# Optimization experiments

Hardware: AMD Instinct MI355X
Metric: run time of the kernel (lower is better)

Reference implementation:

```python
import jax, jax.numpy as jnp
import numpy as np

N = 50000      # nodes
E = 800000     # edges (avg degree 16)
D = 64         # input/hidden dim
OUT = 1        # output head dim
ATT_SLOPE = 0.2   # PyG GATConv leaky_relu slope for attention logits
ACT_SLOPE = 0.01  # nn.LeakyReLU default slope


def _gat_layer(x, src, dst, W, a_src, a_dst, b, n):
    """PyG GATConv, heads=1, concat=True, with self-loops already in src/dst."""
    h = x @ W.T                                   # [n, D]
    logit = jax.nn.leaky_relu(h[src] @ a_src + h[dst] @ a_dst, ATT_SLOPE)  # [e]
    m = jax.ops.segment_max(logit, dst, num_segments=n)                    # per-dst max
    e = jnp.exp(logit - m[dst])
    denom = jax.ops.segment_sum(e, dst, num_segments=n)
    coef = e / denom[dst]                         # softmax over incoming edges
    out = jax.ops.segment_sum(coef[:, None] * h[src], dst, num_segments=n)
    return out + b


def setup_inputs() -> dict:
    key = jax.random.key(0)
    ks = jax.random.split(key, 16)
    s = 1.0 / np.sqrt(D)
    inp = {"x": jax.random.normal(ks[0], (N, D), dtype=jnp.float32)}
    for i in range(3):
        inp[f"W{i}"] = jax.random.normal(ks[1 + 4 * i], (D, D), dtype=jnp.float32) * s
        inp[f"a_src{i}"] = jax.random.normal(ks[2 + 4 * i], (D,), dtype=jnp.float32) * s
        inp[f"a_dst{i}"] = jax.random.normal(ks[3 + 4 * i], (D,), dtype=jnp.float32) * s
        inp[f"b{i}"] = jnp.zeros((D,), dtype=jnp.float32)
    inp["Wout"] = jax.random.normal(ks[13], (OUT, D), dtype=jnp.float32) * s
    inp["bout"] = jnp.zeros((OUT,), dtype=jnp.float32)
    inp["edge_index"] = jax.random.randint(ks[14], (2, E), 0, N, dtype=jnp.int64)
    return inp


def reference(x, W0, a_src0, a_dst0, b0, W1, a_src1, a_dst1, b1,
              W2, a_src2, a_dst2, b2, Wout, bout, edge_index):
    n = x.shape[0]
    loops = jnp.arange(n, dtype=edge_index.dtype)
    src = jnp.concatenate([edge_index[0], loops])  # GATConv add_self_loops=True
    dst = jnp.concatenate([edge_index[1], loops])
    act = lambda v: jax.nn.leaky_relu(v, ACT_SLOPE)
    h = act(_gat_layer(x, src, dst, W0, a_src0, a_dst0, b0, n))
    h = act(_gat_layer(h, src, dst, W1, a_src1, a_dst1, b1, n))
    h = act(_gat_layer(h, src, dst, W2, a_src2, a_dst2, b2, n))
    return h @ Wout.T + bout                       # [n, OUT]
```

## Files before the change

kernel.cpp:

```cpp
#include <hip/hip_runtime.h>
#include <hip/hip_fp16.h>

#define DD 64
#define ATT_SLOPE 0.2f
#define ACT_SLOPE 0.01f
#define GNPB 32
#define RCAP 64
#define PA_CHUNK 2048
#define BSH 8
#define BNODES 256
#define BCAP 5888

template <bool IN_HALF>
__device__ __forceinline__ void gemm_body(
        const void* __restrict__ in_, const float* __restrict__ W,
        const float* __restrict__ a_src, const float* __restrict__ a_dst,
        __half* __restrict__ h, float* __restrict__ as_out,
        float* __restrict__ ad_out, int n_nodes, int base, float* xin) {
    int t = threadIdx.x;
    int lane = t & 63;
    int w = t >> 6;
    if (IN_HALF) {
        const uint2* src = (const uint2*)in_;
        float4* xin4 = (float4*)xin;
        int lim = n_nodes * (DD / 4);
        #pragma unroll
        for (int i = 0; i < 2; ++i) {
            int idx = i * 256 + t;
            int gi = base * (DD / 4) + idx;
            uint2 v = {0, 0};
            if (gi < lim) v = src[gi];
            float2 f0 = __half22float2(*(const __half2*)&v.x);
            float2 f1 = __half22float2(*(const __half2*)&v.y);
            xin4[idx] = make_float4(f0.x, f0.y, f1.x, f1.y);
        }
    } else {
        float4* xin4 = (float4*)xin;
        const float4* src4 = (const float4*)in_;
        int lim = n_nodes * (DD / 4);
        #pragma unroll
        for (int i = 0; i < (GNPB * DD / 4) / 256; ++i) {
            int idx = i * 256 + t;
            int gi = base * (DD / 4) + idx;
            xin4[idx] = (gi < lim) ? src4[gi]
                                   : make_float4(0.f, 0.f, 0.f, 0.f);
        }
    }
    __syncthreads();

    int n0 = base + w * 8;
    if (n0 >= n_nodes) return;

    float asl = a_src[lane], adl = a_dst[lane];
    const float* wrow = W + (size_t)lane * 64;
    int rmax = n_nodes - n0; if (rmax > 8) rmax = 8;

    if (rmax == 8) {
        float a[8] = {0.f, 0.f, 0.f, 0.f, 0.f, 0.f, 0.f, 0.f};
        #pragma unroll
        for (int kq = 0; kq < 16; ++kq) {
            float4 wv = *(const float4*)(wrow + kq * 4);
            #pragma unroll
            for (int r = 0; r < 8; ++r) {
                float4 xv = *(const float4*)&xin[(w * 8 + r) * DD + kq * 4];
                a[r] = fmaf(xv.x, wv.x, a[r]); a[r] = fmaf(xv.y, wv.y, a[r]);
                a[r] = fmaf(xv.z, wv.z, a[r]); a[r] = fmaf(xv.w, wv.w, a[r]);
            }
        }
        #pragma unroll
        for (int r = 0; r < 8; ++r)
            h[(size_t)(n0 + r) * 64 + lane] = __float2half(a[r]);
        float s[16];
        #pragma unroll
        for (int r = 0; r < 8; ++r) { s[2 * r] = a[r] * asl; s[2 * r + 1] = a[r] * adl; }
        #pragma unroll
        for (int m = 32; m >= 1; m >>= 1) {
            #pragma unroll
            for (int i = 0; i < 16; ++i) s[i] += __shfl_xor(s[i], m, 64);
        }
        if (lane == 0) {
            #pragma unroll
            for (int r = 0; r < 8; ++r) {
                as_out[n0 + r] = s[2 * r];
                ad_out[n0 + r] = s[2 * r + 1];
            }
        }
    } else {
        for (int r = 0; r < rmax; ++r) {
            int node = n0 + r;
            float acc = 0.f;
            #pragma unroll
            for (int kq = 0; kq < 16; ++kq) {
                float4 wv = *(const float4*)(wrow + kq * 4);
                float4 xv = *(const float4*)&xin[(w * 8 + r) * DD + kq * 4];
                acc = fmaf(xv.x, wv.x, acc); acc = fmaf(xv.y, wv.y, acc);
                acc = fmaf(xv.z, wv.z, acc); acc = fmaf(xv.w, wv.w, acc);
            }
            h[(size_t)node * 64 + lane] = __float2half(acc);
            float s1 = acc * asl, s2 = acc * adl;
            #pragma unroll
            for (int m = 32; m >= 1; m >>= 1) {
                s1 += __shfl_xor(s1, m, 64);
                s2 += __shfl_xor(s2, m, 64);
            }
            if (lane == 0) { as_out[node] = s1; ad_out[node] = s2; }
        }
    }
}

__global__ __launch_bounds__(256) void gemm0_binA_kernel(
        const float* __restrict__ x, const float* __restrict__ W,
        const float* __restrict__ a_src, const float* __restrict__ a_dst,
        __half* __restrict__ h, float* __restrict__ as_out,
        float* __restrict__ ad_out, int n_nodes,
        const int* __restrict__ ei, int E,
        int* __restrict__ bcur, unsigned int* __restrict__ bucket_buf,
        int bin_blocks) {
    __shared__ float xin[GNPB * DD];
    int* hist  = (int*)xin;
    int* gbase = hist + 256;
    int bid = blockIdx.x;
    if (bid >= bin_blocks) {
        gemm_body<false>(x, W, a_src, a_dst, h, as_out, ad_out, n_nodes,
                         (bid - bin_blocks) * GNPB, xin);
        return;
    }
    int t = threadIdx.x;
    int base_e = bid * PA_CHUNK;
    int ET = E + n_nodes;
    hist[t] = 0;
    __syncthreads();

    unsigned int ent[8];
    short eb[8];
    short ep[8];
    #pragma unroll
    for (int j = 0; j < 8; ++j) {
        int e = base_e + j * 256 + t;
        eb[j] = -1;
        if (e >= ET) continue;
        int s, d;
        if (e < E) { s = ei[e]; d = ei[E + e]; }
        else       { s = e - E; d = s; }
        int b = d >> BSH;
        ent[j] = (unsigned int)s | ((unsigned int)(d & (BNODES - 1)) << 16);
        eb[j] = (short)b;
        ep[j] = (short)atomicAdd(&hist[b], 1);
    }
    __syncthreads();
    {
        int c = hist[t];
        gbase[t] = (c > 0) ? atomicAdd(&bcur[t], c) : 0;
    }
    __syncthreads();
    #pragma unroll
    for (int j = 0; j < 8; ++j) {
        if (eb[j] < 0) continue;
        int pos = gbase[eb[j]] + ep[j];
        if (pos < BCAP) bucket_buf[(size_t)eb[j] * BCAP + pos] = ent[j];
    }
}

__global__ __launch_bounds__(256) void binB_kernel(
        const unsigned int* __restrict__ bucket_buf, const int* __restrict__ bcur,
        int* __restrict__ counts, unsigned short* __restrict__ col_src,
        int n_nodes) {
    __shared__ int cur[BNODES];
    int b = blockIdx.x, t = threadIdx.x;
    if (t < BNODES) cur[t] = 0;
    __syncthreads();
    int cnt = bcur[b]; if (cnt > BCAP) cnt = BCAP;
    const unsigned int* buf = bucket_buf + (size_t)b * BCAP;
    for (int i = t; i < cnt; i += 256) {
        unsigned int en = buf[i];
        int s = en & 0xFFFF;
        int dl = en >> 16;
        int pos = atomicAdd(&cur[dl], 1);
        if (pos < RCAP)
            col_src[(((b << BSH) + dl) << 6) + pos] = (unsigned short)s;
    }
    __syncthreads();
    int n0 = b << BSH;
    if (t < BNODES) {
        int d = n0 + t;
        if (d < n_nodes) counts[d] = cur[t];
    }
}

__global__ __launch_bounds__(256) void gemm_alpha_kernel(
        const __half* __restrict__ in, const float* __restrict__ W,
        const float* __restrict__ a_src, const float* __restrict__ a_dst,
        __half* __restrict__ h, float* __restrict__ as_out,
        float* __restrict__ ad_out, int n_nodes) {
    __shared__ float xin[GNPB * DD];
    gemm_body<true>(in, W, a_src, a_dst, h, as_out, ad_out, n_nodes,
                    blockIdx.x * GNPB, xin);
}

template <bool FUSE_HEAD>
__global__ __launch_bounds__(256) void aggregate_kernel(
        const int* __restrict__ counts, const unsigned short* __restrict__ col_src,
        const __half* __restrict__ h, const float* __restrict__ as_arr,
        const float* __restrict__ ad_arr, const float* __restrict__ b,
        __half* __restrict__ out16, float* __restrict__ head_out,
        const float* __restrict__ Wout, const float* __restrict__ bout,
        int n_nodes) {
    int t = threadIdx.x;
    int lane = t & 63;
    int w = t >> 6;
    int g = lane >> 3, u = lane & 7;
    int node = blockIdx.x * GNPB + w * 8 + g;
    bool valid = node < n_nodes;

    int cnt = 0; float adn = 0.f;
    if (valid) { cnt = counts[node]; adn = ad_arr[node]; }
    if (cnt > RCAP) cnt = RCAP;
    const unsigned short* crow = col_src + ((size_t)node << 6);

    float acc[8] = {0.f, 0.f, 0.f, 0.f, 0.f, 0.f, 0.f, 0.f};
    float lsum = 0.f;

    int nb = (cnt + 7) >> 3;
    uint4 iv = make_uint4(0, 0, 0, 0);
    if (cnt > 0) iv = *(const uint4*)crow;

    for (int bi = 0; bi < nb; ++bi) {
        uint4 ivn = make_uint4(0, 0, 0, 0);
        if (bi + 1 < nb) ivn = *(const uint4*)(crow + (bi + 1) * 8);
        int rem = cnt - (bi << 3); if (rem > 8) rem = 8;

        int s0 = iv.x & 0xFFFF, s1 = iv.x >> 16;
        int s2 = iv.y & 0xFFFF, s3 = iv.y >> 16;
        int s4 = iv.z & 0xFFFF, s5 = iv.z >> 16;
        int s6 = iv.w & 0xFFFF, s7 = iv.w >> 16;
        int ss0 = s0, ss1 = s1, ss2 = s2, ss3 = s3;
        int ss4 = s4, ss5 = s5, ss6 = s6, ss7 = s7;

        uint4 r0={0,0,0,0},r1={0,0,0,0},r2={0,0,0,0},r3={0,0,0,0};
        uint4 r4={0,0,0,0},r5={0,0,0,0},r6={0,0,0,0},r7={0,0,0,0};
        float a0=0,a1=0,a2=0,a3=0,a4=0,a5=0,a6=0,a7=0;
        if (0 < rem) { a0 = as_arr[ss0]; r0 = *(const uint4*)(h + (size_t)ss0 * 64 + u * 8); }
        if (1 < rem) { a1 = as_arr[ss1]; r1 = *(const uint4*)(h + (size_t)ss1 * 64 + u * 8); }
        if (2 < rem) { a2 = as_arr[ss2]; r2 = *(const uint4*)(h + (size_t)ss2 * 64 + u * 8); }
        if (3 < rem) { a3 = as_arr[ss3]; r3 = *(const uint4*)(h + (size_t)ss3 * 64 + u * 8); }
        if (4 < rem) { a4 = as_arr[ss4]; r4 = *(const uint4*)(h + (size_t)ss4 * 64 + u * 8); }
        if (5 < rem) { a5 = as_arr[ss5]; r5 = *(const uint4*)(h + (size_t)ss5 * 64 + u * 8); }
        if (6 < rem) { a6 = as_arr[ss6]; r6 = *(const uint4*)(h + (size_t)ss6 * 64 + u * 8); }
        if (7 < rem) { a7 = as_arr[ss7]; r7 = *(const uint4*)(h + (size_t)ss7 * 64 + u * 8); }

        #define PROC(i, ri, ai)                                              \
        if (i < rem) {                                                       \
            float lg = ai + adn;                                             \
            lg = (lg >= 0.f) ? lg : ATT_SLOPE * lg;                          \
            float p = __expf(lg);                                            \
            lsum += p;                                                       \
            float2 f0 = __half22float2(*(const __half2*)&ri.x);              \
            float2 f1 = __half22float2(*(const __half2*)&ri.y);              \
            float2 f2 = __half22float2(*(const __half2*)&ri.z);              \
            float2 f3 = __half22float2(*(const __half2*)&ri.w);              \
            acc[0] = fmaf(p, f0.x, acc[0]); acc[1] = fmaf(p, f0.y, acc[1]);  \
            acc[2] = fmaf(p, f1.x, acc[2]); acc[3] = fmaf(p, f1.y, acc[3]);  \
            acc[4] = fmaf(p, f2.x, acc[4]); acc[5] = fmaf(p, f2.y, acc[5]);  \
            acc[6] = fmaf(p, f3.x, acc[6]); acc[7] = fmaf(p, f3.y, acc[7]);  \
        }
        PROC(0, r0, a0) PROC(1, r1, a1) PROC(2, r2, a2) PROC(3, r3, a3)
        PROC(4, r4, a4) PROC(5, r5, a5) PROC(6, r6, a6) PROC(7, r7, a7)
        #undef PROC
        iv = ivn;
    }

    float inv = 1.f / lsum;
    const float4 b0 = *(const float4*)(b + u * 8);
    const float4 b1 = *(const float4*)(b + u * 8 + 4);
    float o[8];
    o[0] = acc[0] * inv + b0.x; o[1] = acc[1] * inv + b0.y;
    o[2] = acc[2] * inv + b0.z; o[3] = acc[3] * inv + b0.w;
    o[4] = acc[4] * inv + b1.x; o[5] = acc[5] * inv + b1.y;
    o[6] = acc[6] * inv + b1.z; o[7] = acc[7] * inv + b1.w;
    #pragma unroll
    for (int i = 0; i < 8; ++i) o[i] = (o[i] >= 0.f) ? o[i] : ACT_SLOPE * o[i];

    if (FUSE_HEAD) {
        const float4 w0 = *(const float4*)(Wout + u * 8);
        const float4 w1 = *(const float4*)(Wout + u * 8 + 4);
        float pd = o[0] * w0.x + o[1] * w0.y + o[2] * w0.z + o[3] * w0.w
                 + o[4] * w1.x + o[5] * w1.y + o[6] * w1.z + o[7] * w1.w;
        pd += __shfl_xor(pd, 1, 64);
        pd += __shfl_xor(pd, 2, 64);
        pd += __shfl_xor(pd, 4, 64);
        if (valid && u == 0) head_out[node] = pd + bout[0];
    } else if (valid) {
        __half2 p0 = __floats2half2_rn(o[0], o[1]);
        __half2 p1 = __floats2half2_rn(o[2], o[3]);
        __half2 p2 = __floats2half2_rn(o[4], o[5]);
        __half2 p3 = __floats2half2_rn(o[6], o[7]);
        uint4 pv;
        pv.x = *(unsigned int*)&p0; pv.y = *(unsigned int*)&p1;
        pv.z = *(unsigned int*)&p2; pv.w = *(unsigned int*)&p3;
        *(uint4*)(out16 + ((size_t)node << 6) + u * 8) = pv;
    }
}


extern "C" void kernel_launch(void* const* d_in, const int* in_sizes, int n_in,
                              void* d_out, int out_size, void* d_ws, size_t ws_size,
                              hipStream_t stream) {
    const float* x     = (const float*)d_in[0];
    const float* W[3]  = {(const float*)d_in[1], (const float*)d_in[5], (const float*)d_in[9]};
    const float* as[3] = {(const float*)d_in[2], (const float*)d_in[6], (const float*)d_in[10]};
    const float* ad[3] = {(const float*)d_in[3], (const float*)d_in[7], (const float*)d_in[11]};
    const float* bv[3] = {(const float*)d_in[4], (const float*)d_in[8], (const float*)d_in[12]};
    const float* Wout  = (const float*)d_in[13];
    const float* bout  = (const float*)d_in[14];
    const int*   ei    = (const int*)d_in[15];

    const int N  = in_sizes[0] / DD;
    const int E  = in_sizes[15] / 2;
    const int ET = E + N;
    const int NBUCK = (N + BNODES - 1) >> BSH;

    char* ws = (char*)d_ws;
    size_t off = 0;
    auto alloc = [&](size_t bytes) {
        void* p = ws + off;
        off = (off + bytes + 255) & ~(size_t)255;
        return p;
    };
    unsigned short* col_src = (unsigned short*)alloc((size_t)N * RCAP * 2);
    int*    counts  = (int*)alloc((size_t)N * 4);
    int*    bcur    = (int*)alloc(256 * 4);
    float*  asA     = (float*)alloc((size_t)N * 4);
    float*  adA     = (float*)alloc((size_t)N * 4);
    float*  asB     = (float*)alloc((size_t)N * 4);
    float*  adB     = (float*)alloc((size_t)N * 4);
    __half* hA      = (__half*)alloc((size_t)N * DD * 2);
    __half* hB      = (__half*)alloc((size_t)N * DD * 2);
    __half* obuf16  = (__half*)alloc((size_t)N * DD * 2);
    unsigned int* bucket_buf = (unsigned int*)alloc((size_t)NBUCK * BCAP * 4);
    (void)ws_size;

    int gridG = (N + GNPB - 1) / GNPB;
    int nA    = (ET + PA_CHUNK - 1) / PA_CHUNK;

    hipMemsetAsync(bcur, 0, 256 * 4, stream);
    gemm0_binA_kernel<<<gridG + nA, 256, 0, stream>>>(
        x, W[0], as[0], ad[0], hA, asA, adA, N,
        ei, E, bcur, bucket_buf, nA);
    binB_kernel<<<NBUCK, 256, 0, stream>>>(bucket_buf, bcur, counts, col_src, N);

    aggregate_kernel<false><<<gridG, 256, 0, stream>>>(
        counts, col_src, hA, asA, adA, bv[0], obuf16,
        nullptr, nullptr, nullptr, N);
    gemm_alpha_kernel<<<gridG, 256, 0, stream>>>(obuf16, W[1], as[1], ad[1],
                                                 hB, asB, adB, N);
    aggregate_kernel<false><<<gridG, 256, 0, stream>>>(
        counts, col_src, hB, asB, adB, bv[1], obuf16,
        nullptr, nullptr, nullptr, N);
    gemm_alpha_kernel<<<gridG, 256, 0, stream>>>(obuf16, W[2], as[2], ad[2],
                                                 hA, asA, adA, N);
    aggregate_kernel<true><<<gridG, 256, 0, stream>>>(
        counts, col_src, hA, asA, adA, bv[2], nullptr,
        (float*)d_out, Wout, bout, N);
}
```

Baseline: 244.8 us.

## Fuse all GAT layers into one persistent cooperative kernel with grid syncs

Replaces the seven separate kernel launches (binning, GEMMs, aggregations) with one cooperative persistent kernel. Its blocks loop over tiles for each stage and use grid-wide syncs between stages. The aim is to remove launch overhead and inter-kernel gaps between the short stages. In exchange, occupancy is capped at the co-resident block count, and the aggregation stages lose the latency hiding that full-size grids with many more blocks provided.

```diff
diff --git a/kernel.cpp b/kernel.cpp
--- a/kernel.cpp
+++ b/kernel.cpp
@@ -1,5 +1,8 @@
 #include <hip/hip_runtime.h>
 #include <hip/hip_fp16.h>
+#include <hip/hip_cooperative_groups.h>
+
+namespace cg = cooperative_groups;
 
 #define DD 64
 #define ATT_SLOPE 0.2f
@@ -11,8 +14,9 @@
 #define BNODES 256
 #define BCAP 5888
 
+
 template <bool IN_HALF>
-__device__ __forceinline__ void gemm_body(
+__device__ __forceinline__ void gemm_tile(
         const void* __restrict__ in_, const float* __restrict__ W,
         const float* __restrict__ a_src, const float* __restrict__ a_dst,
         __half* __restrict__ h, float* __restrict__ as_out,
@@ -49,84 +53,74 @@
     __syncthreads();
 
     int n0 = base + w * 8;
-    if (n0 >= n_nodes) return;
-
-    float asl = a_src[lane], adl = a_dst[lane];
-    const float* wrow = W + (size_t)lane * 64;
-    int rmax = n_nodes - n0; if (rmax > 8) rmax = 8;
-
-    if (rmax == 8) {
-        float a[8] = {0.f, 0.f, 0.f, 0.f, 0.f, 0.f, 0.f, 0.f};
-        #pragma unroll
-        for (int kq = 0; kq < 16; ++kq) {
-            float4 wv = *(const float4*)(wrow + kq * 4);
-            #pragma unroll
-            for (int r = 0; r < 8; ++r) {
-                float4 xv = *(const float4*)&xin[(w * 8 + r) * DD + kq * 4];
-                a[r] = fmaf(xv.x, wv.x, a[r]); a[r] = fmaf(xv.y, wv.y, a[r]);
-                a[r] = fmaf(xv.z, wv.z, a[r]); a[r] = fmaf(xv.w, wv.w, a[r]);
-            }
-        }
-        #pragma unroll
-        for (int r = 0; r < 8; ++r)
-            h[(size_t)(n0 + r) * 64 + lane] = __float2half(a[r]);
-        float s[16];
-        #pragma unroll
-        for (int r = 0; r < 8; ++r) { s[2 * r] = a[r] * asl; s[2 * r + 1] = a[r] * adl; }
-        #pragma unroll
-        for (int m = 32; m >= 1; m >>= 1) {
-            #pragma unroll
-            for (int i = 0; i < 16; ++i) s[i] += __shfl_xor(s[i], m, 64);
-        }
-        if (lane == 0) {
-            #pragma unroll
-            for (int r = 0; r < 8; ++r) {
-                as_out[n0 + r] = s[2 * r];
-                ad_out[n0 + r] = s[2 * r + 1];
-            }
-        }
-    } else {
-        for (int r = 0; r < rmax; ++r) {
-            int node = n0 + r;
-            float acc = 0.f;
+    if (n0 < n_nodes) {
+        float asl = a_src[lane], adl = a_dst[lane];
+        const float* wrow = W + (size_t)lane * 64;
+        int rmax = n_nodes - n0; if (rmax > 8) rmax = 8;
+
+        if (rmax == 8) {
+            float a[8] = {0.f, 0.f, 0.f, 0.f, 0.f, 0.f, 0.f, 0.f};
             #pragma unroll
             for (int kq = 0; kq < 16; ++kq) {
                 float4 wv = *(const float4*)(wrow + kq * 4);
-                float4 xv = *(const float4*)&xin[(w * 8 + r) * DD + kq * 4];
-                acc = fmaf(xv.x, wv.x, acc); acc = fmaf(xv.y, wv.y, acc);
-                acc = fmaf(xv.z, wv.z, acc); acc = fmaf(xv.w, wv.w, acc);
+                #pragma unroll
+                for (int r = 0; r < 8; ++r) {
+                    float4 xv = *(const float4*)&xin[(w * 8 + r) * DD + kq * 4];
+                    a[r] = fmaf(xv.x, wv.x, a[r]); a[r] = fmaf(xv.y, wv.y, a[r]);
+                    a[r] = fmaf(xv.z, wv.z, a[r]); a[r] = fmaf(xv.w, wv.w, a[r]);
+                }
             }
-            h[(size_t)node * 64 + lane] = __float2half(acc);
-            float s1 = acc * asl, s2 = acc * adl;
+            #pragma unroll
+            for (int r = 0; r < 8; ++r)
+                h[(size_t)(n0 + r) * 64 + lane] = __float2half(a[r]);
+            float s[16];
+            #pragma unroll
+            for (int r = 0; r < 8; ++r) { s[2*r] = a[r] * asl; s[2*r+1] = a[r] * adl; }
             #pragma unroll
             for (int m = 32; m >= 1; m >>= 1) {
-                s1 += __shfl_xor(s1, m, 64);
-                s2 += __shfl_xor(s2, m, 64);
+                #pragma unroll
+                for (int i = 0; i < 16; ++i) s[i] += __shfl_xor(s[i], m, 64);
             }
-            if (lane == 0) { as_out[node] = s1; ad_out[node] = s2; }
+            if (lane == 0) {
+                #pragma unroll
+                for (int r = 0; r < 8; ++r) {
+                    as_out[n0 + r] = s[2 * r];
+                    ad_out[n0 + r] = s[2 * r + 1];
+                }
+            }
+        } else {
+            for (int r = 0; r < rmax; ++r) {
+                int node = n0 + r;
+                float acc = 0.f;
+                #pragma unroll
+                for (int kq = 0; kq < 16; ++kq) {
+                    float4 wv = *(const float4*)(wrow + kq * 4);
+                    float4 xv = *(const float4*)&xin[(w * 8 + r) * DD + kq * 4];
+                    acc = fmaf(xv.x, wv.x, acc); acc = fmaf(xv.y, wv.y, acc);
+                    acc = fmaf(xv.z, wv.z, acc); acc = fmaf(xv.w, wv.w, acc);
+                }
+                h[(size_t)node * 64 + lane] = __float2half(acc);
+                float s1 = acc * asl, s2 = acc * adl;
+                #pragma unroll
+                for (int m = 32; m >= 1; m >>= 1) {
+                    s1 += __shfl_xor(s1, m, 64);
+                    s2 += __shfl_xor(s2, m, 64);
+                }
+                if (lane == 0) { as_out[node] = s1; ad_out[node] = s2; }
+            }
         }
     }
-}
-
-__global__ __launch_bounds__(256) void gemm0_binA_kernel(
-        const float* __restrict__ x, const float* __restrict__ W,
-        const float* __restrict__ a_src, const float* __restrict__ a_dst,
-        __half* __restrict__ h, float* __restrict__ as_out,
-        float* __restrict__ ad_out, int n_nodes,
-        const int* __restrict__ ei, int E,
+    __syncthreads();
+}
+
+__device__ __forceinline__ void binA_task(
+        const int* __restrict__ ei, int E, int n_nodes,
         int* __restrict__ bcur, unsigned int* __restrict__ bucket_buf,
-        int bin_blocks) {
-    __shared__ float xin[GNPB * DD];
+        int chunk, float* xin) {
     int* hist  = (int*)xin;
     int* gbase = hist + 256;
-    int bid = blockIdx.x;
-    if (bid >= bin_blocks) {
-        gemm_body<false>(x, W, a_src, a_dst, h, as_out, ad_out, n_nodes,
-                         (bid - bin_blocks) * GNPB, xin);
-        return;
-    }
     int t = threadIdx.x;
-    int base_e = bid * PA_CHUNK;
+    int base_e = chunk * PA_CHUNK;
     int ET = E + n_nodes;
     hist[t] = 0;
     __syncthreads();
@@ -159,15 +153,16 @@
         int pos = gbase[eb[j]] + ep[j];
         if (pos < BCAP) bucket_buf[(size_t)eb[j] * BCAP + pos] = ent[j];
     }
-}
-
-__global__ __launch_bounds__(256) void binB_kernel(
+    __syncthreads();
+}
+
+__device__ __forceinline__ void binB_task(
         const unsigned int* __restrict__ bucket_buf, const int* __restrict__ bcur,
         int* __restrict__ counts, unsigned short* __restrict__ col_src,
-        int n_nodes) {
-    __shared__ int cur[BNODES];
-    int b = blockIdx.x, t = threadIdx.x;
-    if (t < BNODES) cur[t] = 0;
+        int n_nodes, int b, float* xin) {
+    int* cur = (int*)xin;
+    int t = threadIdx.x;
+    cur[t] = 0;
     __syncthreads();
     int cnt = bcur[b]; if (cnt > BCAP) cnt = BCAP;
     const unsigned int* buf = bucket_buf + (size_t)b * BCAP;
@@ -181,35 +176,26 @@
     }
     __syncthreads();
     int n0 = b << BSH;
-    if (t < BNODES) {
+    {
         int d = n0 + t;
         if (d < n_nodes) counts[d] = cur[t];
     }
-}
-
-__global__ __launch_bounds__(256) void gemm_alpha_kernel(
-        const __half* __restrict__ in, const float* __restrict__ W,
-        const float* __restrict__ a_src, const float* __restrict__ a_dst,
-        __half* __restrict__ h, float* __restrict__ as_out,
-        float* __restrict__ ad_out, int n_nodes) {
-    __shared__ float xin[GNPB * DD];
-    gemm_body<true>(in, W, a_src, a_dst, h, as_out, ad_out, n_nodes,
-                    blockIdx.x * GNPB, xin);
+    __syncthreads();
 }
 
 template <bool FUSE_HEAD>
-__global__ __launch_bounds__(256) void aggregate_kernel(
+__device__ __forceinline__ void agg_tile(
         const int* __restrict__ counts, const unsigned short* __restrict__ col_src,
         const __half* __restrict__ h, const float* __restrict__ as_arr,
         const float* __restrict__ ad_arr, const float* __restrict__ b,
         __half* __restrict__ out16, float* __restrict__ head_out,
         const float* __restrict__ Wout, const float* __restrict__ bout,
-        int n_nodes) {
+        int n_nodes, int tile) {
     int t = threadIdx.x;
     int lane = t & 63;
     int w = t >> 6;
     int g = lane >> 3, u = lane & 7;
-    int node = blockIdx.x * GNPB + w * 8 + g;
+    int node = tile * GNPB + w * 8 + g;
     bool valid = node < n_nodes;
 
     int cnt = 0; float adn = 0.f;
@@ -229,12 +215,10 @@
         if (bi + 1 < nb) ivn = *(const uint4*)(crow + (bi + 1) * 8);
         int rem = cnt - (bi << 3); if (rem > 8) rem = 8;
 
-        int s0 = iv.x & 0xFFFF, s1 = iv.x >> 16;
-        int s2 = iv.y & 0xFFFF, s3 = iv.y >> 16;
-        int s4 = iv.z & 0xFFFF, s5 = iv.z >> 16;
-        int s6 = iv.w & 0xFFFF, s7 = iv.w >> 16;
-        int ss0 = s0, ss1 = s1, ss2 = s2, ss3 = s3;
-        int ss4 = s4, ss5 = s5, ss6 = s6, ss7 = s7;
+        int ss0 = iv.x & 0xFFFF, ss1 = iv.x >> 16;
+        int ss2 = iv.y & 0xFFFF, ss3 = iv.y >> 16;
+        int ss4 = iv.z & 0xFFFF, ss5 = iv.z >> 16;
+        int ss6 = iv.w & 0xFFFF, ss7 = iv.w >> 16;
 
         uint4 r0={0,0,0,0},r1={0,0,0,0},r2={0,0,0,0},r3={0,0,0,0};
         uint4 r4={0,0,0,0},r5={0,0,0,0},r6={0,0,0,0},r7={0,0,0,0};
@@ -301,22 +285,91 @@
     }
 }
 
+__global__ __launch_bounds__(256, 4) void gnn_persistent(
+        const float* __restrict__ x,
+        const float* __restrict__ W0, const float* __restrict__ as0,
+        const float* __restrict__ ad0, const float* __restrict__ b0,
+        const float* __restrict__ W1, const float* __restrict__ as1,
+        const float* __restrict__ ad1, const float* __restrict__ b1,
+        const float* __restrict__ W2, const float* __restrict__ as2,
+        const float* __restrict__ ad2, const float* __restrict__ b2,
+        const float* __restrict__ Wout, const float* __restrict__ bout,
+        const int* __restrict__ ei, int E, int n_nodes,
+        int* bcur, unsigned int* bucket_buf,
+        int* counts, unsigned short* col_src,
+        float* asA, float* adA, float* asB, float* adB,
+        __half* hA, __half* hB, __half* obuf16,
+        float* head_out) {
+    __shared__ float xin[GNPB * DD];
+    cg::grid_group grid = cg::this_grid();
+    const int nbk   = gridDim.x;
+    const int bid   = blockIdx.x;
+    const int gridG = (n_nodes + GNPB - 1) / GNPB;
+    const int nA    = (E + n_nodes + PA_CHUNK - 1) / PA_CHUNK;
+    const int NBUCK = (n_nodes + BNODES - 1) >> BSH;
+
+    int tasks0 = nA + gridG;
+    for (int task = bid; task < tasks0; task += nbk) {
+        if (task < nA)
+            binA_task(ei, E, n_nodes, bcur, bucket_buf, task, xin);
+        else
+            gemm_tile<false>(x, W0, as0, ad0, hA, asA, adA, n_nodes,
+                             (task - nA) * GNPB, xin);
+    }
+    grid.sync();
+
+    for (int bkt = bid; bkt < NBUCK; bkt += nbk)
+        binB_task(bucket_buf, bcur, counts, col_src, n_nodes, bkt, xin);
+    grid.sync();
+
+    for (int tile = bid; tile < gridG; tile += nbk)
+        agg_tile<false>(counts, col_src, hA, asA, adA, b0, obuf16,
+                        nullptr, nullptr, nullptr, n_nodes, tile);
+    grid.sync();
+
+    for (int tile = bid; tile < gridG; tile += nbk)
+        gemm_tile<true>(obuf16, W1, as1, ad1, hB, asB, adB, n_nodes,
+                        tile * GNPB, xin);
+    grid.sync();
+
+    for (int tile = bid; tile < gridG; tile += nbk)
+        agg_tile<false>(counts, col_src, hB, asB, adB, b1, obuf16,
+                        nullptr, nullptr, nullptr, n_nodes, tile);
+    grid.sync();
+
+    for (int tile = bid; tile < gridG; tile += nbk)
+        gemm_tile<true>(obuf16, W2, as2, ad2, hA, asA, adA, n_nodes,
+                        tile * GNPB, xin);
+    grid.sync();
+
+    for (int tile = bid; tile < gridG; tile += nbk)
+        agg_tile<true>(counts, col_src, hA, asA, adA, b2,
+                       nullptr, head_out, Wout, bout, n_nodes, tile);
+}
+
 
 extern "C" void kernel_launch(void* const* d_in, const int* in_sizes, int n_in,
                               void* d_out, int out_size, void* d_ws, size_t ws_size,
                               hipStream_t stream) {
     const float* x     = (const float*)d_in[0];
-    const float* W[3]  = {(const float*)d_in[1], (const float*)d_in[5], (const float*)d_in[9]};
-    const float* as[3] = {(const float*)d_in[2], (const float*)d_in[6], (const float*)d_in[10]};
-    const float* ad[3] = {(const float*)d_in[3], (const float*)d_in[7], (const float*)d_in[11]};
-    const float* bv[3] = {(const float*)d_in[4], (const float*)d_in[8], (const float*)d_in[12]};
+    const float* W0    = (const float*)d_in[1];
+    const float* as0   = (const float*)d_in[2];
+    const float* ad0   = (const float*)d_in[3];
+    const float* b0    = (const float*)d_in[4];
+    const float* W1    = (const float*)d_in[5];
+    const float* as1   = (const float*)d_in[6];
+    const float* ad1   = (const float*)d_in[7];
+    const float* b1    = (const float*)d_in[8];
+    const float* W2    = (const float*)d_in[9];
+    const float* as2   = (const float*)d_in[10];
+    const float* ad2   = (const float*)d_in[11];
+    const float* b2    = (const float*)d_in[12];
     const float* Wout  = (const float*)d_in[13];
     const float* bout  = (const float*)d_in[14];
     const int*   ei    = (const int*)d_in[15];
 
-    const int N  = in_sizes[0] / DD;
-    const int E  = in_sizes[15] / 2;
-    const int ET = E + N;
+    int N  = in_sizes[0] / DD;
+    int E  = in_sizes[15] / 2;
     const int NBUCK = (N + BNODES - 1) >> BSH;
 
     char* ws = (char*)d_ws;
@@ -337,28 +390,43 @@
     __half* hB      = (__half*)alloc((size_t)N * DD * 2);
     __half* obuf16  = (__half*)alloc((size_t)N * DD * 2);
     unsigned int* bucket_buf = (unsigned int*)alloc((size_t)NBUCK * BCAP * 4);
+    float* head_out = (float*)d_out;
     (void)ws_size;
 
     int gridG = (N + GNPB - 1) / GNPB;
-    int nA    = (ET + PA_CHUNK - 1) / PA_CHUNK;
+    int nA    = (E + N + PA_CHUNK - 1) / PA_CHUNK;
+    int tasks0 = nA + gridG;
+
+    static int capBlocks = 0;
+    if (capBlocks == 0) {
+        int nbPerCU = 0;
+        hipOccupancyMaxActiveBlocksPerMultiprocessor(
+            &nbPerCU, (const void*)gnn_persistent, 256, 0);
+        if (nbPerCU < 1) nbPerCU = 1;
+        int dev = 0;
+        hipGetDevice(&dev);
+        hipDeviceProp_t prop;
+        hipGetDeviceProperties(&prop, dev);
+        int cus = prop.multiProcessorCount > 0 ? prop.multiProcessorCount : 256;
+        capBlocks = nbPerCU * cus;
+    }
+    int grid = tasks0 < capBlocks ? tasks0 : capBlocks;
 
     hipMemsetAsync(bcur, 0, 256 * 4, stream);
-    gemm0_binA_kernel<<<gridG + nA, 256, 0, stream>>>(
-        x, W[0], as[0], ad[0], hA, asA, adA, N,
-        ei, E, bcur, bucket_buf, nA);
-    binB_kernel<<<NBUCK, 256, 0, stream>>>(bucket_buf, bcur, counts, col_src, N);
-
-    aggregate_kernel<false><<<gridG, 256, 0, stream>>>(
-        counts, col_src, hA, asA, adA, bv[0], obuf16,
-        nullptr, nullptr, nullptr, N);
-    gemm_alpha_kernel<<<gridG, 256, 0, stream>>>(obuf16, W[1], as[1], ad[1],
-                                                 hB, asB, adB, N);
-    aggregate_kernel<false><<<gridG, 256, 0, stream>>>(
-        counts, col_src, hB, asB, adB, bv[1], obuf16,
-        nullptr, nullptr, nullptr, N);
-    gemm_alpha_kernel<<<gridG, 256, 0, stream>>>(obuf16, W[2], as[2], ad[2],
-                                                 hA, asA, adA, N);
-    aggregate_kernel<true><<<gridG, 256, 0, stream>>>(
-        counts, col_src, hA, asA, adA, bv[2], nullptr,
-        (float*)d_out, Wout, bout, N);
-}
+
+    void* args[] = {
+        (void*)&x,
+        (void*)&W0, (void*)&as0, (void*)&ad0, (void*)&b0,
+        (void*)&W1, (void*)&as1, (void*)&ad1, (void*)&b1,
+        (void*)&W2, (void*)&as2, (void*)&ad2, (void*)&b2,
+        (void*)&Wout, (void*)&bout,
+        (void*)&ei, (void*)&E, (void*)&N,
+        (void*)&bcur, (void*)&bucket_buf,
+        (void*)&counts, (void*)&col_src,
+        (void*)&asA, (void*)&adA, (void*)&asB, (void*)&adB,
+        (void*)&hA, (void*)&hB, (void*)&obuf16,
+        (void*)&head_out
+    };
+    hipLaunchCooperativeKernel((const void*)gnn_persistent,
+                               dim3(grid), dim3(256), args, 0, stream);
+}
```

New measurement: 644.7 us. 163% more time.

## Fuse aggregation with next layer's linear transform and attention projections

Applied to the files above, without the earlier changes.

Merges each intermediate aggregate kernel with the following GEMM+alpha kernel. The aggregated node features go straight into shared memory and feed the next layer's W multiply, so the fp16 intermediate buffer is neither written nor re-read. This also drops two kernel launches. The fused kernel keeps features in fp32 instead of rounding to half between stages, and it may raise register pressure or lower occupancy in the aggregation phase.

```diff
diff --git a/kernel.cpp b/kernel.cpp
--- a/kernel.cpp
+++ b/kernel.cpp
@@ -11,40 +11,24 @@
 #define BNODES 256
 #define BCAP 5888
 
-template <bool IN_HALF>
-__device__ __forceinline__ void gemm_body(
-        const void* __restrict__ in_, const float* __restrict__ W,
+
+__device__ __forceinline__ void gemm_body0(
+        const float* __restrict__ in, const float* __restrict__ W,
         const float* __restrict__ a_src, const float* __restrict__ a_dst,
         __half* __restrict__ h, float* __restrict__ as_out,
         float* __restrict__ ad_out, int n_nodes, int base, float* xin) {
     int t = threadIdx.x;
     int lane = t & 63;
     int w = t >> 6;
-    if (IN_HALF) {
-        const uint2* src = (const uint2*)in_;
-        float4* xin4 = (float4*)xin;
-        int lim = n_nodes * (DD / 4);
-        #pragma unroll
-        for (int i = 0; i < 2; ++i) {
-            int idx = i * 256 + t;
-            int gi = base * (DD / 4) + idx;
-            uint2 v = {0, 0};
-            if (gi < lim) v = src[gi];
-            float2 f0 = __half22float2(*(const __half2*)&v.x);
-            float2 f1 = __half22float2(*(const __half2*)&v.y);
-            xin4[idx] = make_float4(f0.x, f0.y, f1.x, f1.y);
-        }
-    } else {
-        float4* xin4 = (float4*)xin;
-        const float4* src4 = (const float4*)in_;
-        int lim = n_nodes * (DD / 4);
-        #pragma unroll
-        for (int i = 0; i < (GNPB * DD / 4) / 256; ++i) {
-            int idx = i * 256 + t;
-            int gi = base * (DD / 4) + idx;
-            xin4[idx] = (gi < lim) ? src4[gi]
-                                   : make_float4(0.f, 0.f, 0.f, 0.f);
-        }
+    float4* xin4 = (float4*)xin;
+    const float4* src4 = (const float4*)in;
+    int lim = n_nodes * (DD / 4);
+    #pragma unroll
+    for (int i = 0; i < (GNPB * DD / 4) / 256; ++i) {
+        int idx = i * 256 + t;
+        int gi = base * (DD / 4) + idx;
+        xin4[idx] = (gi < lim) ? src4[gi]
+                               : make_float4(0.f, 0.f, 0.f, 0.f);
     }
     __syncthreads();
 
@@ -121,8 +105,8 @@
     int* gbase = hist + 256;
     int bid = blockIdx.x;
     if (bid >= bin_blocks) {
-        gemm_body<false>(x, W, a_src, a_dst, h, as_out, ad_out, n_nodes,
-                         (bid - bin_blocks) * GNPB, xin);
+        gemm_body0(x, W, a_src, a_dst, h, as_out, ad_out, n_nodes,
+                   (bid - bin_blocks) * GNPB, xin);
         return;
     }
     int t = threadIdx.x;
@@ -187,31 +171,12 @@
     }
 }
 
-__global__ __launch_bounds__(256) void gemm_alpha_kernel(
-        const __half* __restrict__ in, const float* __restrict__ W,
-        const float* __restrict__ a_src, const float* __restrict__ a_dst,
-        __half* __restrict__ h, float* __restrict__ as_out,
-        float* __restrict__ ad_out, int n_nodes) {
-    __shared__ float xin[GNPB * DD];
-    gemm_body<true>(in, W, a_src, a_dst, h, as_out, ad_out, n_nodes,
-                    blockIdx.x * GNPB, xin);
-}
-
-template <bool FUSE_HEAD>
-__global__ __launch_bounds__(256) void aggregate_kernel(
+__device__ __forceinline__ bool agg_core(
         const int* __restrict__ counts, const unsigned short* __restrict__ col_src,
         const __half* __restrict__ h, const float* __restrict__ as_arr,
         const float* __restrict__ ad_arr, const float* __restrict__ b,
-        __half* __restrict__ out16, float* __restrict__ head_out,
-        const float* __restrict__ Wout, const float* __restrict__ bout,
-        int n_nodes) {
-    int t = threadIdx.x;
-    int lane = t & 63;
-    int w = t >> 6;
-    int g = lane >> 3, u = lane & 7;
-    int node = blockIdx.x * GNPB + w * 8 + g;
+        int n_nodes, int node, int u, float o[8]) {
     bool valid = node < n_nodes;
-
     int cnt = 0; float adn = 0.f;
     if (valid) { cnt = counts[node]; adn = ad_arr[node]; }
     if (cnt > RCAP) cnt = RCAP;
@@ -229,12 +194,10 @@
         if (bi + 1 < nb) ivn = *(const uint4*)(crow + (bi + 1) * 8);
         int rem = cnt - (bi << 3); if (rem > 8) rem = 8;
 
-        int s0 = iv.x & 0xFFFF, s1 = iv.x >> 16;
-        int s2 = iv.y & 0xFFFF, s3 = iv.y >> 16;
-        int s4 = iv.z & 0xFFFF, s5 = iv.z >> 16;
-        int s6 = iv.w & 0xFFFF, s7 = iv.w >> 16;
-        int ss0 = s0, ss1 = s1, ss2 = s2, ss3 = s3;
-        int ss4 = s4, ss5 = s5, ss6 = s6, ss7 = s7;
+        int ss0 = iv.x & 0xFFFF, ss1 = iv.x >> 16;
+        int ss2 = iv.y & 0xFFFF, ss3 = iv.y >> 16;
+        int ss4 = iv.z & 0xFFFF, ss5 = iv.z >> 16;
+        int ss6 = iv.w & 0xFFFF, ss7 = iv.w >> 16;
 
         uint4 r0={0,0,0,0},r1={0,0,0,0},r2={0,0,0,0},r3={0,0,0,0};
         uint4 r4={0,0,0,0},r5={0,0,0,0},r6={0,0,0,0},r7={0,0,0,0};
@@ -272,33 +235,123 @@
     float inv = 1.f / lsum;
     const float4 b0 = *(const float4*)(b + u * 8);
     const float4 b1 = *(const float4*)(b + u * 8 + 4);
-    float o[8];
     o[0] = acc[0] * inv + b0.x; o[1] = acc[1] * inv + b0.y;
     o[2] = acc[2] * inv + b0.z; o[3] = acc[3] * inv + b0.w;
     o[4] = acc[4] * inv + b1.x; o[5] = acc[5] * inv + b1.y;
     o[6] = acc[6] * inv + b1.z; o[7] = acc[7] * inv + b1.w;
     #pragma unroll
     for (int i = 0; i < 8; ++i) o[i] = (o[i] >= 0.f) ? o[i] : ACT_SLOPE * o[i];
-
-    if (FUSE_HEAD) {
-        const float4 w0 = *(const float4*)(Wout + u * 8);
-        const float4 w1 = *(const float4*)(Wout + u * 8 + 4);
-        float pd = o[0] * w0.x + o[1] * w0.y + o[2] * w0.z + o[3] * w0.w
-                 + o[4] * w1.x + o[5] * w1.y + o[6] * w1.z + o[7] * w1.w;
-        pd += __shfl_xor(pd, 1, 64);
-        pd += __shfl_xor(pd, 2, 64);
-        pd += __shfl_xor(pd, 4, 64);
-        if (valid && u == 0) head_out[node] = pd + bout[0];
-    } else if (valid) {
-        __half2 p0 = __floats2half2_rn(o[0], o[1]);
-        __half2 p1 = __floats2half2_rn(o[2], o[3]);
-        __half2 p2 = __floats2half2_rn(o[4], o[5]);
-        __half2 p3 = __floats2half2_rn(o[6], o[7]);
-        uint4 pv;
-        pv.x = *(unsigned int*)&p0; pv.y = *(unsigned int*)&p1;
-        pv.z = *(unsigned int*)&p2; pv.w = *(unsigned int*)&p3;
-        *(uint4*)(out16 + ((size_t)node << 6) + u * 8) = pv;
-    }
+    return valid;
+}
+
+__global__ __launch_bounds__(256) void fused_agg_gemm_kernel(
+        const int* __restrict__ counts, const unsigned short* __restrict__ col_src,
+        const __half* __restrict__ h, const float* __restrict__ as_arr,
+        const float* __restrict__ ad_arr, const float* __restrict__ b,
+        const float* __restrict__ Wn, const float* __restrict__ an_src,
+        const float* __restrict__ an_dst, __half* __restrict__ h_next,
+        float* __restrict__ as_next, float* __restrict__ ad_next,
+        int n_nodes) {
+    __shared__ float xin[GNPB * DD];
+    int t = threadIdx.x;
+    int lane = t & 63;
+    int w = t >> 6;
+    int g = lane >> 3, u = lane & 7;
+    int node = blockIdx.x * GNPB + w * 8 + g;
+
+    float o[8];
+    bool valid = agg_core(counts, col_src, h, as_arr, ad_arr, b,
+                          n_nodes, node, u, o);
+    if (valid) {
+        float4* row = (float4*)&xin[(w * 8 + g) * DD + u * 8];
+        row[0] = make_float4(o[0], o[1], o[2], o[3]);
+        row[1] = make_float4(o[4], o[5], o[6], o[7]);
+    }
+    __syncthreads();
+
+    int n0 = blockIdx.x * GNPB + w * 8;
+    if (n0 >= n_nodes) return;
+    float asl = an_src[lane], adl = an_dst[lane];
+    const float* wrow = Wn + (size_t)lane * 64;
+    int rmax = n_nodes - n0; if (rmax > 8) rmax = 8;
+
+    if (rmax == 8) {
+        float a[8] = {0.f, 0.f, 0.f, 0.f, 0.f, 0.f, 0.f, 0.f};
+        #pragma unroll
+        for (int kq = 0; kq < 16; ++kq) {
+            float4 wv = *(const float4*)(wrow + kq * 4);
+            #pragma unroll
+            for (int r = 0; r < 8; ++r) {
+                float4 xv = *(const float4*)&xin[(w * 8 + r) * DD + kq * 4];
+                a[r] = fmaf(xv.x, wv.x, a[r]); a[r] = fmaf(xv.y, wv.y, a[r]);
+                a[r] = fmaf(xv.z, wv.z, a[r]); a[r] = fmaf(xv.w, wv.w, a[r]);
+            }
+        }
+        #pragma unroll
+        for (int r = 0; r < 8; ++r)
+            h_next[(size_t)(n0 + r) * 64 + lane] = __float2half(a[r]);
+        float s[16];
+        #pragma unroll
+        for (int r = 0; r < 8; ++r) { s[2 * r] = a[r] * asl; s[2 * r + 1] = a[r] * adl; }
+        #pragma unroll
+        for (int m = 32; m >= 1; m >>= 1) {
+            #pragma unroll
+            for (int i = 0; i < 16; ++i) s[i] += __shfl_xor(s[i], m, 64);
+        }
+        if (lane == 0) {
+            #pragma unroll
+            for (int r = 0; r < 8; ++r) {
+                as_next[n0 + r] = s[2 * r];
+                ad_next[n0 + r] = s[2 * r + 1];
+            }
+        }
+    } else {
+        for (int r = 0; r < rmax; ++r) {
+            int nd = n0 + r;
+            float acc = 0.f;
+            #pragma unroll
+            for (int kq = 0; kq < 16; ++kq) {
+                float4 wv = *(const float4*)(wrow + kq * 4);
+                float4 xv = *(const float4*)&xin[(w * 8 + r) * DD + kq * 4];
+                acc = fmaf(xv.x, wv.x, acc); acc = fmaf(xv.y, wv.y, acc);
+                acc = fmaf(xv.z, wv.z, acc); acc = fmaf(xv.w, wv.w, acc);
+            }
+            h_next[(size_t)nd * 64 + lane] = __float2half(acc);
+            float s1 = acc * asl, s2 = acc * adl;
+            #pragma unroll
+            for (int m = 32; m >= 1; m >>= 1) {
+                s1 += __shfl_xor(s1, m, 64);
+                s2 += __shfl_xor(s2, m, 64);
+            }
+            if (lane == 0) { as_next[nd] = s1; ad_next[nd] = s2; }
+        }
+    }
+}
+
+__global__ __launch_bounds__(256) void aggregate_head_kernel(
+        const int* __restrict__ counts, const unsigned short* __restrict__ col_src,
+        const __half* __restrict__ h, const float* __restrict__ as_arr,
+        const float* __restrict__ ad_arr, const float* __restrict__ b,
+        float* __restrict__ head_out, const float* __restrict__ Wout,
+        const float* __restrict__ bout, int n_nodes) {
+    int t = threadIdx.x;
+    int lane = t & 63;
+    int w = t >> 6;
+    int g = lane >> 3, u = lane & 7;
+    int node = blockIdx.x * GNPB + w * 8 + g;
+
+    float o[8];
+    bool valid = agg_core(counts, col_src, h, as_arr, ad_arr, b,
+                          n_nodes, node, u, o);
+
+    const float4 w0 = *(const float4*)(Wout + u * 8);
+    const float4 w1 = *(const float4*)(Wout + u * 8 + 4);
+    float pd = o[0] * w0.x + o[1] * w0.y + o[2] * w0.z + o[3] * w0.w
+             + o[4] * w1.x + o[5] * w1.y + o[6] * w1.z + o[7] * w1.w;
+    pd += __shfl_xor(pd, 1, 64);
+    pd += __shfl_xor(pd, 2, 64);
+    pd += __shfl_xor(pd, 4, 64);
+    if (valid && u == 0) head_out[node] = pd + bout[0];
 }
 
 
@@ -335,7 +388,6 @@
     float*  adB     = (float*)alloc((size_t)N * 4);
     __half* hA      = (__half*)alloc((size_t)N * DD * 2);
     __half* hB      = (__half*)alloc((size_t)N * DD * 2);
-    __half* obuf16  = (__half*)alloc((size_t)N * DD * 2);
     unsigned int* bucket_buf = (unsigned int*)alloc((size_t)NBUCK * BCAP * 4);
     (void)ws_size;
 
@@ -348,17 +400,13 @@
         ei, E, bcur, bucket_buf, nA);
     binB_kernel<<<NBUCK, 256, 0, stream>>>(bucket_buf, bcur, counts, col_src, N);
 
-    aggregate_kernel<false><<<gridG, 256, 0, stream>>>(
-        counts, col_src, hA, asA, adA, bv[0], obuf16,
-        nullptr, nullptr, nullptr, N);
-    gemm_alpha_kernel<<<gridG, 256, 0, stream>>>(obuf16, W[1], as[1], ad[1],
-                                                 hB, asB, adB, N);
-    aggregate_kernel<false><<<gridG, 256, 0, stream>>>(
-        counts, col_src, hB, asB, adB, bv[1], obuf16,
-        nullptr, nullptr, nullptr, N);
-    gemm_alpha_kernel<<<gridG, 256, 0, stream>>>(obuf16, W[2], as[2], ad[2],
-                                                 hA, asA, adA, N);
-    aggregate_kernel<true><<<gridG, 256, 0, stream>>>(
-        counts, col_src, hA, asA, adA, bv[2], nullptr,
+    fused_agg_gemm_kernel<<<gridG, 256, 0, stream>>>(
+        counts, col_src, hA, asA, adA, bv[0],
+        W[1], as[1], ad[1], hB, asB, adB, N);
+    fused_agg_gemm_kernel<<<gridG, 256, 0, stream>>>(
+        counts, col_src, hB, asB, adB, bv[1],
+        W[2], as[2], ad[2], hA, asA, adA, N);
+    aggregate_head_kernel<<<gridG, 256, 0, stream>>>(
+        counts, col_src, hA, asA, adA, bv[2],
         (float*)d_out, Wout, bout, N);
 }
```

Result: faster. 228.5 us, median of 2 (-6.7%).
